# Kernel optimization log

Hardware: AMD Instinct MI355X
Metric: run time of the kernel (lower is better)

The kernel has to match this reference:

```python
import jax, jax.numpy as jnp
import numpy as np

D_MODEL = 1024

def setup_inputs() -> dict:
    key = jax.random.key(0)
    ks = jax.random.split(key, 7)
    s = 1.0 / np.sqrt(D_MODEL)
    x = jax.random.normal(ks[0], (4, 2048, D_MODEL), dtype=jnp.float32)
    Wq = jax.random.normal(ks[1], (D_MODEL, D_MODEL), dtype=jnp.float32) * s
    Wk = jax.random.normal(ks[2], (D_MODEL, D_MODEL), dtype=jnp.float32) * s
    Wv = jax.random.normal(ks[3], (D_MODEL, D_MODEL), dtype=jnp.float32) * s
    bq = jax.random.normal(ks[4], (D_MODEL,), dtype=jnp.float32) * 0.01
    bk = jax.random.normal(ks[5], (D_MODEL,), dtype=jnp.float32) * 0.01
    bv = jax.random.normal(ks[6], (D_MODEL,), dtype=jnp.float32) * 0.01
    return {"x": x, "Wq": Wq, "bq": bq, "Wk": Wk, "bk": bk, "Wv": Wv, "bv": bv}

def reference(x, Wq, bq, Wk, bk, Wv, bv):
    # Linear layers: y = x @ W^T + b (torch nn.Linear convention)
    q = jnp.einsum('bsd,ed->bse', x, Wq) + bq
    k = jnp.einsum('bsd,ed->bse', x, Wk) + bk
    v = jnp.einsum('bsd,ed->bse', x, Wv) + bv
    scale = 1.0 / jnp.sqrt(jnp.asarray(k.shape[-1], dtype=x.dtype))
    scores = jnp.einsum('bqd,bkd->bqk', q, k) * scale  # [B, S, S]
    attn = jax.nn.softmax(scores, axis=-1)
    return jnp.einsum('bqk,bkd->bqd', attn, v)
```

## Files before the change

kernel.cpp:

```cpp
#include <hip/hip_runtime.h>
#include <cstdint>


typedef unsigned short u16;
typedef __attribute__((ext_vector_type(4))) float f32x4;
typedef __attribute__((ext_vector_type(8))) __bf16 bf16x8;

#define AS1(p) ((const __attribute__((address_space(1))) void*)(p))
#define AS3(p) ((__attribute__((address_space(3))) void*)(p))

#define SEQ 2048
#define DM 1024

__device__ __forceinline__ u16 f2b(float f) {
  uint32_t u = __builtin_bit_cast(uint32_t, f);
  u += 0x7FFFu + ((u >> 16) & 1u);
  return (u16)(u >> 16);
}
__device__ __forceinline__ float b2f(uint32_t bits16) {
  return __builtin_bit_cast(float, bits16 << 16);
}

__global__ __launch_bounds__(256) void cvt_all(const float* __restrict__ x,
                                               const float* __restrict__ Wq,
                                               const float* __restrict__ Wk,
                                               const float* __restrict__ Wv,
                                               u16* __restrict__ xb,
                                               u16* __restrict__ wcat) {
  const int bid = blockIdx.x;
  const float* src;
  u16* dst;
  int i;
  if (bid < 8192) {
    i = (bid * 256 + threadIdx.x) * 4;
    src = x; dst = xb;
  } else {
    i = ((bid - 8192) * 256 + threadIdx.x) * 4;
    dst = wcat;
    if (i < (1 << 20))      { src = Wq; }
    else if (i < (2 << 20)) { src = Wk; i -= (1 << 20); dst = wcat + (1 << 20); }
    else                    { src = Wv; i -= (2 << 20); dst = wcat + (2 << 20); }
  }
  float4 v = *(const float4*)(src + i);
  ushort4 o;
  o.x = f2b(v.x); o.y = f2b(v.y); o.z = f2b(v.z); o.w = f2b(v.w);
  *(ushort4*)(dst + i) = o;
}

#define BK 64

__device__ __forceinline__ void stage_tile(const u16* __restrict__ g, int ld,
                                           char* lds, int tid) {
  int w = tid >> 6, l = tid & 63;
#pragma unroll
  for (int p = 0; p < 4; ++p) {
    int o  = p * 4096 + w * 1024 + l * 16;
    int r  = o >> 7;
    int pc = (o >> 4) & 7;
    int lc = pc ^ (r & 7);
    const u16* src = g + r * ld + lc * 8;
    char* dst = lds + p * 4096 + w * 1024;
    __builtin_amdgcn_global_load_lds(AS1(src), AS3(dst), 16, 0, 0);
  }
}

__device__ __forceinline__ bf16x8 read_frag(const char* lds, int row, int kk) {
  int lc  = kk >> 3;
  int off = row * 128 + ((lc ^ (row & 7)) << 4);
  return *(const bf16x8*)(lds + off);
}

__device__ __forceinline__ void gemm_core(const u16* __restrict__ A,
                                          const u16* __restrict__ Bt,
                                          int K, int lda, int ldb,
                                          char* ldsA, char* ldsB,
                                          f32x4 acc[4][4], int tid) {
  int w = tid >> 6, l = tid & 63;
  int wm = (w >> 1) * 64, wn = (w & 1) * 64;
  int fr = l & 15, fk = (l >> 4) * 8;
  for (int k0 = 0; k0 < K; k0 += BK) {
    stage_tile(A + k0, lda, ldsA, tid);
    stage_tile(Bt + k0, ldb, ldsB, tid);
    __syncthreads();
#pragma unroll
    for (int ks = 0; ks < 2; ++ks) {
      bf16x8 af[4], bfr[4];
#pragma unroll
      for (int m = 0; m < 4; ++m) af[m]  = read_frag(ldsA, wm + m * 16 + fr, ks * 32 + fk);
#pragma unroll
      for (int n = 0; n < 4; ++n) bfr[n] = read_frag(ldsB, wn + n * 16 + fr, ks * 32 + fk);
#pragma unroll
      for (int m = 0; m < 4; ++m)
#pragma unroll
        for (int n = 0; n < 4; ++n)
          acc[m][n] = __builtin_amdgcn_mfma_f32_16x16x32_bf16(af[m], bfr[n], acc[m][n], 0, 0, 0);
    }
    __syncthreads();
  }
}

#define ZERO_ACC(acc)                                     \
  _Pragma("unroll") for (int m_ = 0; m_ < 4; ++m_)        \
  _Pragma("unroll") for (int n_ = 0; n_ < 4; ++n_)        \
  _Pragma("unroll") for (int j_ = 0; j_ < 4; ++j_)        \
      acc[m_][n_][j_] = 0.f;

__global__ __launch_bounds__(256, 2) void qkv_gemm(const u16* __restrict__ xb,
                                                   const u16* __restrict__ wcat,
                                                   const float* __restrict__ bq,
                                                   const float* __restrict__ bk,
                                                   const float* __restrict__ bv,
                                                   u16* __restrict__ qb,
                                                   u16* __restrict__ kb,
                                                   u16* __restrict__ vtb) {
  __shared__ __align__(16) char lds[32768];
  int tid = threadIdx.x;
  int bm = blockIdx.y * 128, bn = blockIdx.x * 128;
  f32x4 acc[4][4];
  ZERO_ACC(acc);
  gemm_core(xb + bm * 1024, wcat + bn * 1024, 1024, 1024, 1024,
            lds, lds + 16384, acc, tid);
  int w = tid >> 6, l = tid & 63;
  int wm = (w >> 1) * 64, wn = (w & 1) * 64;
  int which = bn >> 10;
  if (which == 2) {
    const float* bias = bv;
#pragma unroll
    for (int m = 0; m < 4; ++m)
#pragma unroll
      for (int n = 0; n < 4; ++n) {
        int col = bn + wn + n * 16 + (l & 15);
        int e = col & 1023;
        float bval = bias[e];
#pragma unroll
        for (int j = 0; j < 4; ++j) {
          int row = bm + wm + m * 16 + (l >> 4) * 4 + j;
          int b = row >> 11, s = row & 2047;
          vtb[(b << 21) + e * 2048 + s] = f2b(acc[m][n][j] + bval);
        }
      }
  } else {
    u16* outp = (which == 0) ? qb : kb;
    const float* bias = (which == 0) ? bq : bk;
    const int ebase = bn & 1023;
    __syncthreads();
#pragma unroll
    for (int m = 0; m < 4; ++m)
#pragma unroll
      for (int n = 0; n < 4; ++n) {
        int cl = wn + n * 16 + (l & 15);
        float bval = bias[ebase + cl];
#pragma unroll
        for (int j = 0; j < 4; ++j) {
          int rl = wm + m * 16 + (l >> 4) * 4 + j;
          int chunk = (cl >> 3) ^ (rl & 7);
          *(u16*)(lds + rl * 256 + chunk * 16 + (cl & 7) * 2) = f2b(acc[m][n][j] + bval);
        }
      }
    __syncthreads();
#pragma unroll
    for (int p = 0; p < 8; ++p) {
      int rl = p * 16 + (tid >> 4);
      int c  = tid & 15;
      int phys = c ^ (rl & 7);
      uint4 v = *(const uint4*)(lds + rl * 256 + phys * 16);
      *(uint4*)(outp + (size_t)(bm + rl) * 1024 + ebase + c * 8) = v;
    }
  }
}

__global__ __launch_bounds__(256, 2) void scores_gemm(const u16* __restrict__ qb,
                                                      const u16* __restrict__ kb,
                                                      u16* __restrict__ pb,
                                                      float* __restrict__ psum) {
  __shared__ __align__(16) char lds[32768];
  int tid = threadIdx.x;
  int b = blockIdx.z;
  int bx = blockIdx.x;
  int bm = blockIdx.y * 128, bn = bx * 128;
  f32x4 acc[4][4];
  ZERO_ACC(acc);
  gemm_core(qb + b * (SEQ * DM) + bm * 1024,
            kb + b * (SEQ * DM) + bn * 1024, 1024, 1024, 1024,
            lds, lds + 16384, acc, tid);
  u16* out = pb + (size_t)b * SEQ * SEQ;
  int w = tid >> 6, l = tid & 63;
  int wm = (w >> 1) * 64, wn = (w & 1) * 64;
  const int wn_i = w & 1;
#pragma unroll
  for (int m = 0; m < 4; ++m)
#pragma unroll
    for (int n = 0; n < 4; ++n)
#pragma unroll
      for (int j = 0; j < 4; ++j)
        acc[m][n][j] = __expf(acc[m][n][j] * 0.03125f - 4.0f);
#pragma unroll
  for (int m = 0; m < 4; ++m)
#pragma unroll
    for (int j = 0; j < 4; ++j) {
      float ps = (acc[m][0][j] + acc[m][1][j]) + (acc[m][2][j] + acc[m][3][j]);
      ps += __shfl_xor(ps, 1);
      ps += __shfl_xor(ps, 2);
      ps += __shfl_xor(ps, 4);
      ps += __shfl_xor(ps, 8);
      if ((l & 15) == 0) {
        int rl = wm + m * 16 + (l >> 4) * 4 + j;
        psum[((size_t)b * SEQ + bm + rl) * 32 + bx * 2 + wn_i] = ps;
      }
    }
  __syncthreads();
#pragma unroll
  for (int m = 0; m < 4; ++m)
#pragma unroll
    for (int n = 0; n < 4; ++n) {
      int cl = wn + n * 16 + (l & 15);
#pragma unroll
      for (int j = 0; j < 4; ++j) {
        int rl = wm + m * 16 + (l >> 4) * 4 + j;
        int chunk = (cl >> 3) ^ (rl & 7);
        *(u16*)(lds + rl * 256 + chunk * 16 + (cl & 7) * 2) = f2b(acc[m][n][j]);
      }
    }
  __syncthreads();
#pragma unroll
  for (int p = 0; p < 8; ++p) {
    int rl = p * 16 + (tid >> 4);
    int c  = tid & 15;
    int phys = c ^ (rl & 7);
    uint4 v = *(const uint4*)(lds + rl * 256 + phys * 16);
    *(uint4*)(out + (size_t)(bm + rl) * 2048 + bn + c * 8) = v;
  }
}

__global__ __launch_bounds__(256, 2) void pv_gemm(const u16* __restrict__ pb,
                                                  const u16* __restrict__ vtb,
                                                  const float* __restrict__ psum,
                                                  float* __restrict__ out) {
  __shared__ __align__(16) char lds[32768];
  __shared__ float inv_s[128];
  int tid = threadIdx.x;
  int b = blockIdx.z;
  int bm = blockIdx.y * 128, bn = blockIdx.x * 128;
  if (tid < 128) {
    const float4* ps = (const float4*)(psum + ((size_t)b * SEQ + bm + tid) * 32);
    float4 s0 = ps[0], s1 = ps[1], s2 = ps[2], s3 = ps[3];
    float4 s4 = ps[4], s5 = ps[5], s6 = ps[6], s7 = ps[7];
    float t = ((s0.x + s0.y + s0.z + s0.w) + (s1.x + s1.y + s1.z + s1.w)) +
              ((s2.x + s2.y + s2.z + s2.w) + (s3.x + s3.y + s3.z + s3.w)) +
              ((s4.x + s4.y + s4.z + s4.w) + (s5.x + s5.y + s5.z + s5.w)) +
              ((s6.x + s6.y + s6.z + s6.w) + (s7.x + s7.y + s7.z + s7.w));
    inv_s[tid] = 1.0f / t;
  }
  f32x4 acc[4][4];
  ZERO_ACC(acc);
  gemm_core(pb  + (size_t)b * SEQ * SEQ + bm * 2048,
            vtb + (size_t)b * DM * SEQ  + bn * 2048, 2048, 2048, 2048,
            lds, lds + 16384, acc, tid);
  float* o = out + (size_t)b * SEQ * DM;
  int w = tid >> 6, l = tid & 63;
  int wm = (w >> 1) * 64, wn = (w & 1) * 64;
#pragma unroll
  for (int h = 0; h < 2; ++h) {
    __syncthreads();
#pragma unroll
    for (int mm = 0; mm < 2; ++mm) {
      int m = 2 * h + mm;
#pragma unroll
      for (int n = 0; n < 4; ++n) {
        int cl = wn + n * 16 + (l & 15);
#pragma unroll
        for (int j = 0; j < 4; ++j) {
          int rl = wm + m * 16 + (l >> 4) * 4 + j;
          int sr = (rl & 31) | ((rl >> 6) << 5);
          int clp = cl ^ (((sr >> 2) & 1) << 4);
          *(float*)(lds + sr * 512 + clp * 4) = acc[m][n][j] * inv_s[rl];
        }
      }
    }
    __syncthreads();
#pragma unroll
    for (int p = 0; p < 8; ++p) {
      int sr  = p * 8 + (tid >> 5);
      int c16 = tid & 31;
      int c16p = c16 ^ (((sr >> 2) & 1) << 2);
      uint4 v = *(const uint4*)(lds + sr * 512 + c16p * 16);
      int grow = (sr & 31) + 32 * h + ((sr >> 5) << 6);
      *(uint4*)(o + (size_t)(bm + grow) * 1024 + bn + c16 * 4) = v;
    }
  }
}

extern "C" void kernel_launch(void* const* d_in, const int* in_sizes, int n_in,
                              void* d_out, int out_size, void* d_ws, size_t ws_size,
                              hipStream_t stream) {
  const float* x  = (const float*)d_in[0];
  const float* Wq = (const float*)d_in[1];
  const float* bq = (const float*)d_in[2];
  const float* Wk = (const float*)d_in[3];
  const float* bk = (const float*)d_in[4];
  const float* Wv = (const float*)d_in[5];
  const float* bv = (const float*)d_in[6];
  float* out = (float*)d_out;

  char* ws = (char*)d_ws;
  u16*   xb   = (u16*)(ws);
  u16*   wcat = (u16*)(ws + 16777216);
  u16*   qb   = (u16*)(ws + 23068672);
  u16*   kb   = (u16*)(ws + 39845888);
  u16*   vtb  = (u16*)(ws + 56623104);
  u16*   pb   = (u16*)(ws + 73400320);
  float* psum = (float*)(ws + 106954752);

  cvt_all<<<11264, 256, 0, stream>>>(x, Wq, Wk, Wv, xb, wcat);
  qkv_gemm<<<dim3(24, 64), 256, 0, stream>>>(xb, wcat, bq, bk, bv, qb, kb, vtb);
  scores_gemm<<<dim3(16, 16, 4), 256, 0, stream>>>(qb, kb, pb, psum);
  pv_gemm<<<dim3(8, 16, 4), 256, 0, stream>>>(pb, vtb, psum, out);
}
```

Before: 168.8 us.

## Use 128-wide K tiles and XCD-aware block remap in PV GEMM

The PV GEMM now stages 128-element K slices (64 KB LDS) instead of 64, which halves the number of barriers per output tile. It also switches to a 1D grid whose block index is remapped so that blocks on the same XCD share P rows and V^T columns, aiming for better L2 reuse. The larger LDS footprint lowers occupancy from 2 blocks per CU. The inverse row-sum buffer now reuses the LDS area after the main loop.

```diff
diff --git a/kernel.cpp b/kernel.cpp
--- a/kernel.cpp
+++ b/kernel.cpp
@@ -99,6 +99,55 @@
   }
 }
 
+__device__ __forceinline__ void stage_tile128(const u16* __restrict__ g, int ld,
+                                              char* lds, int tid) {
+  int w = tid >> 6;
+#pragma unroll
+  for (int p = 0; p < 8; ++p) {
+    int o  = p * 4096 + w * 1024 + (tid & 63) * 16;
+    int r  = o >> 8;
+    int pc = (o >> 4) & 15;
+    int lc = (pc & 8) | ((pc & 7) ^ (r & 7));
+    __builtin_amdgcn_global_load_lds(AS1(g + r * ld + lc * 8),
+        AS3(lds + p * 4096 + w * 1024), 16, 0, 0);
+  }
+}
+
+__device__ __forceinline__ bf16x8 read_frag128(const char* lds, int row, int kk) {
+  int lc   = kk >> 3;
+  int phys = (lc & 8) | ((lc & 7) ^ (row & 7));
+  return *(const bf16x8*)(lds + row * 256 + phys * 16);
+}
+
+__device__ __forceinline__ void gemm_core128(const u16* __restrict__ A,
+                                             const u16* __restrict__ Bt,
+                                             int K, int lda, int ldb,
+                                             char* ldsA, char* ldsB,
+                                             f32x4 acc[4][4], int tid) {
+  int w = tid >> 6, l = tid & 63;
+  int wm = (w >> 1) * 64, wn = (w & 1) * 64;
+  int fr = l & 15, fk = (l >> 4) * 8;
+  for (int k0 = 0; k0 < K; k0 += 128) {
+    stage_tile128(A + k0, lda, ldsA, tid);
+    stage_tile128(Bt + k0, ldb, ldsB, tid);
+    __syncthreads();
+#pragma unroll
+    for (int ks = 0; ks < 4; ++ks) {
+      bf16x8 af[4], bfr[4];
+#pragma unroll
+      for (int m = 0; m < 4; ++m) af[m]  = read_frag128(ldsA, wm + m * 16 + fr, ks * 32 + fk);
+#pragma unroll
+      for (int n = 0; n < 4; ++n) bfr[n] = read_frag128(ldsB, wn + n * 16 + fr, ks * 32 + fk);
+#pragma unroll
+      for (int m = 0; m < 4; ++m)
+#pragma unroll
+        for (int n = 0; n < 4; ++n)
+          acc[m][n] = __builtin_amdgcn_mfma_f32_16x16x32_bf16(af[m], bfr[n], acc[m][n], 0, 0, 0);
+    }
+    __syncthreads();
+  }
+}
+
 #define ZERO_ACC(acc)                                     \
   _Pragma("unroll") for (int m_ = 0; m_ < 4; ++m_)        \
   _Pragma("unroll") for (int n_ = 0; n_ < 4; ++n_)        \
@@ -236,26 +285,31 @@
                                                   const u16* __restrict__ vtb,
                                                   const float* __restrict__ psum,
                                                   float* __restrict__ out) {
-  __shared__ __align__(16) char lds[32768];
-  __shared__ float inv_s[128];
+  __shared__ __align__(16) char lds[65536];
   int tid = threadIdx.x;
-  int b = blockIdx.z;
-  int bm = blockIdx.y * 128, bn = blockIdx.x * 128;
+  const int lin = blockIdx.x;
+  const int wgid = (lin & 7) * 64 + (lin >> 3);
+  const int b  = wgid >> 7;
+  const int r  = wgid & 127;
+  const int bn = (r >> 4) * 128;
+  const int bm = (r & 15) * 128;
+  float rowsum = 0.f;
   if (tid < 128) {
     const float4* ps = (const float4*)(psum + ((size_t)b * SEQ + bm + tid) * 32);
     float4 s0 = ps[0], s1 = ps[1], s2 = ps[2], s3 = ps[3];
     float4 s4 = ps[4], s5 = ps[5], s6 = ps[6], s7 = ps[7];
-    float t = ((s0.x + s0.y + s0.z + s0.w) + (s1.x + s1.y + s1.z + s1.w)) +
-              ((s2.x + s2.y + s2.z + s2.w) + (s3.x + s3.y + s3.z + s3.w)) +
-              ((s4.x + s4.y + s4.z + s4.w) + (s5.x + s5.y + s5.z + s5.w)) +
-              ((s6.x + s6.y + s6.z + s6.w) + (s7.x + s7.y + s7.z + s7.w));
-    inv_s[tid] = 1.0f / t;
+    rowsum = ((s0.x + s0.y + s0.z + s0.w) + (s1.x + s1.y + s1.z + s1.w)) +
+             ((s2.x + s2.y + s2.z + s2.w) + (s3.x + s3.y + s3.z + s3.w)) +
+             ((s4.x + s4.y + s4.z + s4.w) + (s5.x + s5.y + s5.z + s5.w)) +
+             ((s6.x + s6.y + s6.z + s6.w) + (s7.x + s7.y + s7.z + s7.w));
   }
   f32x4 acc[4][4];
   ZERO_ACC(acc);
-  gemm_core(pb  + (size_t)b * SEQ * SEQ + bm * 2048,
-            vtb + (size_t)b * DM * SEQ  + bn * 2048, 2048, 2048, 2048,
-            lds, lds + 16384, acc, tid);
+  gemm_core128(pb  + (size_t)b * SEQ * SEQ + bm * 2048,
+               vtb + (size_t)b * DM * SEQ  + bn * 2048, 2048, 2048, 2048,
+               lds, lds + 32768, acc, tid);
+  float* invp = (float*)(lds + 32768);
+  if (tid < 128) invp[tid] = 1.0f / rowsum;
   float* o = out + (size_t)b * SEQ * DM;
   int w = tid >> 6, l = tid & 63;
   int wm = (w >> 1) * 64, wn = (w & 1) * 64;
@@ -273,7 +327,7 @@
           int rl = wm + m * 16 + (l >> 4) * 4 + j;
           int sr = (rl & 31) | ((rl >> 6) << 5);
           int clp = cl ^ (((sr >> 2) & 1) << 4);
-          *(float*)(lds + sr * 512 + clp * 4) = acc[m][n][j] * inv_s[rl];
+          *(float*)(lds + sr * 512 + clp * 4) = acc[m][n][j] * invp[rl];
         }
       }
     }
@@ -314,5 +368,5 @@
   cvt_all<<<11264, 256, 0, stream>>>(x, Wq, Wk, Wv, xb, wcat);
   qkv_gemm<<<dim3(24, 64), 256, 0, stream>>>(xb, wcat, bq, bk, bv, qb, kb, vtb);
   scores_gemm<<<dim3(16, 16, 4), 256, 0, stream>>>(qb, kb, pb, psum);
-  pv_gemm<<<dim3(8, 16, 4), 256, 0, stream>>>(pb, vtb, psum, out);
-}
+  pv_gemm<<<512, 256, 0, stream>>>(pb, vtb, psum, out);
+}
```

After: 157.1 us. -6.9%, faster.
